# Kernel optimization log

Hardware: AMD Instinct MI355X
Metric: run time of the kernel (lower is better)

The kernel has to match this reference:

```python
import jax, jax.numpy as jnp
import numpy as np

B, H, S, D = 4, 16, 2048, 64
ROPE_BASE = 10000.0


def _rope(x):
    # Rotate-half RoPE over the last dim, positions along the second-to-last dim.
    d = x.shape[-1]
    s = x.shape[-2]
    inv_freq = 1.0 / (ROPE_BASE ** (jnp.arange(0, d, 2, dtype=jnp.float32) / d))  # [D/2]
    ang = jnp.arange(s, dtype=jnp.float32)[:, None] * inv_freq                    # [S, D/2]
    cos, sin = jnp.cos(ang), jnp.sin(ang)
    x1, x2 = x[..., : d // 2], x[..., d // 2:]
    return jnp.concatenate([x1 * cos - x2 * sin, x1 * sin + x2 * cos], axis=-1).astype(x.dtype)


def setup_inputs() -> dict:
    key = jax.random.key(0)
    kq, kk, kv = jax.random.split(key, 3)
    q = jax.random.normal(kq, (B, H, S, D), dtype=jnp.float32)
    k = jax.random.normal(kk, (B, H, S, D), dtype=jnp.float32)
    v = jax.random.normal(kv, (B, H, S, D), dtype=jnp.float32)
    mask = jnp.tril(jnp.ones((S, S), dtype=bool))  # causal, broadcasts over [B,H,S,S]
    return {"q": q, "k": k, "v": v, "mask": mask}


def reference(q, k, v, mask):
    d_k = q.shape[-1]
    qr = _rope(q)
    kr = _rope(k)
    scores = jnp.einsum('bhqd,bhkd->bhqk', qr, kr) / jnp.sqrt(jnp.asarray(d_k, jnp.float32))
    scores = jnp.where(mask, scores, -jnp.inf)  # masked_fill(mask == False, -inf)
    probs = jax.nn.softmax(scores, axis=-1)
    return jnp.einsum('bhqk,bhkd->bhqd', probs, v)
```

## Files before the change

### kernel.cpp

```cpp
#include <hip/hip_runtime.h>
#include <hip/hip_bf16.h>
#include <math.h>

#define SS 2048
#define DD 64
#define BH 64
#define KT 64
#define NT 256
#define NKT (SS / KT)
#define QTT 256
#define NTA 512
#define NQT (SS / QTT)
#define LQ 72
#define LOG2E 1.4426950408889634f
#define IFS (13.287712379549449f / 32.0f)

typedef __attribute__((ext_vector_type(8))) short s8v;
typedef __attribute__((ext_vector_type(4))) short s4v;
typedef __attribute__((ext_vector_type(4))) float f4v;

__device__ __forceinline__ short f2b(float x) {
  __hip_bfloat16 h = __float2bfloat16(x);
  return *reinterpret_cast<short*>(&h);
}

__device__ __forceinline__ void gload16(const void* g, void* l) {
  __builtin_amdgcn_global_load_lds(
      (const __attribute__((address_space(1))) void*)g,
      (__attribute__((address_space(3))) void*)l, 16, 0, 0);
}

template <int CTRL>
__device__ __forceinline__ float dppf(float x) {
  int i = __builtin_bit_cast(int, x);
  i = __builtin_amdgcn_update_dpp(i, i, CTRL, 0xf, 0xf, false);
  return __builtin_bit_cast(float, i);
}
__device__ __forceinline__ float rowmax16(float x) {
  x = fmaxf(x, dppf<0xB1>(x));
  x = fmaxf(x, dppf<0x4E>(x));
  x = fmaxf(x, dppf<0x124>(x));
  x = fmaxf(x, dppf<0x128>(x));
  return x;
}
__device__ __forceinline__ float rowsum16(float x) {
  x += dppf<0xB1>(x);
  x += dppf<0x4E>(x);
  x += dppf<0x124>(x);
  x += dppf<0x128>(x);
  return x;
}

__device__ __forceinline__ void rope_cs(int pos, int j, float& c, float& s) {
  float inv = exp2f(-(float)j * IFS);
  float ang = (float)pos * inv;
  __sincosf(ang, &s, &c);
}

__global__ __launch_bounds__(NT) void prep_kv_kernel(
    const float* __restrict__ kg, const float* __restrict__ vg,
    short* __restrict__ kr, short* __restrict__ vt) {
  __shared__ float Vs[KT][DD + 1];
  const int b = blockIdx.x;
  const int kt = b & 31;
  const int t = threadIdx.x;
  const size_t ofs = (size_t)b * (KT * DD);
  const float* ktile = kg + ofs;
  short* krt = kr + ofs;

#pragma unroll
  for (int i = 0; i < 8; ++i) {
    int idx = t + i * NT;
    int r = idx >> 5, j = idx & 31;
    float s, c;
    rope_cs(kt * KT + r, j, c, s);
    float x1 = ktile[r * DD + j], x2 = ktile[r * DD + j + 32];
    krt[r * DD + j] = f2b(x1 * c - x2 * s);
    krt[r * DD + j + 32] = f2b(x1 * s + x2 * c);
  }

  const float* vtile = vg + ofs;
#pragma unroll
  for (int i = 0; i < 4; ++i) {
    int s4 = t + i * NT;
    int r = s4 >> 4, c4 = (s4 & 15) * 4;
    float4 v = *(const float4*)&vtile[r * DD + c4];
    Vs[r][c4 + 0] = v.x;
    Vs[r][c4 + 1] = v.y;
    Vs[r][c4 + 2] = v.z;
    Vs[r][c4 + 3] = v.w;
  }
  __syncthreads();
  short* otile = vt + ofs;
#pragma unroll
  for (int i = 0; i < 2; ++i) {
    int c = t + i * NT;
    int d = c >> 3, k8 = (c & 7) * 8;
    s8v o;
#pragma unroll
    for (int u = 0; u < 8; ++u) {
      int kp = k8 + u;
      int src = ((kp & 3) << 4) + (kp >> 2);
      o[u] = f2b(Vs[src][d]);
    }
    *(s8v*)&otile[d * KT + k8] = o;
  }
}

__global__ __launch_bounds__(NTA, 4) void attn_fast(
    const float* __restrict__ qg, const short* __restrict__ kr,
    const short* __restrict__ vt, float* __restrict__ og) {
  __shared__ __align__(16) short Ks[2][KT * DD];
  __shared__ __align__(16) short Vts[2][DD * KT];
  __shared__ __align__(16) short QP[QTT * DD];

  const int tid = threadIdx.x;
  const int lane = tid & 63;
  const int wv = tid >> 6;
  const int quad = lane >> 4;
  const int lx = lane & 15;
  const int xb = lx & 7;
  const int foff0 = ((quad ^ xb) << 3);
  const int foff1 = (((quad | 4) ^ xb) << 3);

  const int bid = blockIdx.x;
  const int g = bid >> 6;
  const int qb = (g < 4) ? (7 - g) : (g - 4);
  const int bh = bid & 63;
  const int qbase = qb * QTT;
  const int ktmax = 4 * qb + 3;
  const int mykt = 4 * qb + (wv >> 1);
  const float* Q = qg + (size_t)bh * SS * DD;
  float* O = og + (size_t)bh * SS * DD;
  const short* krh = kr + (size_t)bh * SS * DD;
  const short* vth = vt + (size_t)bh * SS * DD;

  const int r_dma = tid >> 3;
  const int qs_dma = (tid & 7) ^ (r_dma & 7);
  const int goff = r_dma * DD + qs_dma * 8;
  const int loff = wv * 512;

  gload16(krh + goff, &Ks[0][loff]);
  gload16(vth + goff, &Vts[0][loff]);

  const float qscale = 0.125f * LOG2E;
#pragma unroll
  for (int t = 0; t < 16; ++t) {
    int idx = tid + t * NTA;
    int r = idx >> 5, j = idx & 31;
    float s, c;
    rope_cs(qbase + r, j, c, s);
    float x1 = Q[(size_t)(qbase + r) * DD + j];
    float x2 = Q[(size_t)(qbase + r) * DD + j + 32];
    int rb = r & 7;
    QP[r * DD + ((((j >> 3) ^ rb) << 3) | (j & 7))] = f2b((x1 * c - x2 * s) * qscale);
    QP[r * DD + (((((j >> 3) | 4) ^ rb) << 3) | (j & 7))] = f2b((x1 * s + x2 * c) * qscale);
  }
  __syncthreads();

  s8v qf0[2], qf1[2];
#pragma unroll
  for (int h = 0; h < 2; ++h) {
    const int rq = wv * 32 + h * 16 + lx;
    qf0[h] = *(const s8v*)&QP[rq * DD + foff0];
    qf1[h] = *(const s8v*)&QP[rq * DD + foff1];
  }

  const short bone = f2b(1.0f);
  s8v ones;
#pragma unroll
  for (int u = 0; u < 8; ++u) ones[u] = bone;

  short* Ps = &QP[wv * 32 * DD];

  f4v o_[2][4];
  f4v ol[2];
#pragma unroll
  for (int h = 0; h < 2; ++h) {
    ol[h] = (f4v){0.f, 0.f, 0.f, 0.f};
#pragma unroll
    for (int db = 0; db < 4; ++db) o_[h][db] = (f4v){0.f, 0.f, 0.f, 0.f};
  }

  for (int kt = 0; kt <= ktmax; ++kt) {
    const int cur = kt & 1;
    if (kt) __syncthreads();

    if (kt < ktmax) {
      const short* ktile = krh + (size_t)(kt + 1) * (KT * DD);
      const short* vtile = vth + (size_t)(kt + 1) * (DD * KT);
      const int nxt = cur ^ 1;
      gload16(ktile + goff, &Ks[nxt][loff]);
      gload16(vtile + goff, &Vts[nxt][loff]);
    }

    if (kt <= mykt) {
      f4v sc[2][4];
#pragma unroll
      for (int nb = 0; nb < 4; ++nb) {
        const int rk = nb * 16 + lx;
        s8v kf0 = *(const s8v*)&Ks[cur][rk * DD + foff0];
        s8v kf1 = *(const s8v*)&Ks[cur][rk * DD + foff1];
#pragma unroll
        for (int h = 0; h < 2; ++h) {
          f4v z = (f4v){0.f, 0.f, 0.f, 0.f};
          z = __builtin_amdgcn_mfma_f32_16x16x32_bf16(qf0[h], kf0, z, 0, 0, 0);
          z = __builtin_amdgcn_mfma_f32_16x16x32_bf16(qf1[h], kf1, z, 0, 0, 0);
          sc[h][nb] = z;
        }
      }

      if (kt == mykt) {
        const int kb = kt * KT;
#pragma unroll
        for (int h = 0; h < 2; ++h) {
          const int qrow = qbase + wv * 32 + h * 16 + quad * 4;
#pragma unroll
          for (int nb = 0; nb < 4; ++nb)
#pragma unroll
            for (int r = 0; r < 4; ++r)
              if (kb + nb * 16 + lx > qrow + r) sc[h][nb][r] = -INFINITY;
        }
      }

#pragma unroll
      for (int h = 0; h < 2; ++h) {
#pragma unroll
        for (int r = 0; r < 4; ++r) {
          const int rl = quad * 4 + r;
          float p0 = __builtin_amdgcn_exp2f(sc[h][0][r]);
          float p1 = __builtin_amdgcn_exp2f(sc[h][1][r]);
          float p2 = __builtin_amdgcn_exp2f(sc[h][2][r]);
          float p3 = __builtin_amdgcn_exp2f(sc[h][3][r]);
          s4v pk = {f2b(p0), f2b(p1), f2b(p2), f2b(p3)};
          *(s4v*)&Ps[(h * 16 + rl) * DD + (((lx >> 1) ^ (rl & 7)) << 3) + ((lx & 1) << 2)] = pk;
        }
      }

      s8v pf0[2], pf1[2];
#pragma unroll
      for (int h = 0; h < 2; ++h) {
        pf0[h] = *(const s8v*)&Ps[(h * 16 + lx) * DD + foff0];
        pf1[h] = *(const s8v*)&Ps[(h * 16 + lx) * DD + foff1];
        ol[h] = __builtin_amdgcn_mfma_f32_16x16x32_bf16(pf0[h], ones, ol[h], 0, 0, 0);
        ol[h] = __builtin_amdgcn_mfma_f32_16x16x32_bf16(pf1[h], ones, ol[h], 0, 0, 0);
      }
#pragma unroll
      for (int db = 0; db < 4; ++db) {
        const int rv = db * 16 + lx;
        s8v vf0 = *(const s8v*)&Vts[cur][rv * KT + foff0];
        s8v vf1 = *(const s8v*)&Vts[cur][rv * KT + foff1];
#pragma unroll
        for (int h = 0; h < 2; ++h) {
          o_[h][db] = __builtin_amdgcn_mfma_f32_16x16x32_bf16(pf0[h], vf0, o_[h][db], 0, 0, 0);
          o_[h][db] = __builtin_amdgcn_mfma_f32_16x16x32_bf16(pf1[h], vf1, o_[h][db], 0, 0, 0);
        }
      }
    }
  }

#pragma unroll
  for (int h = 0; h < 2; ++h)
#pragma unroll
    for (int r = 0; r < 4; ++r) {
      float rinv = 1.0f / ol[h][r];
      int row = qbase + wv * 32 + h * 16 + quad * 4 + r;
#pragma unroll
      for (int db = 0; db < 4; ++db)
        O[(size_t)row * DD + db * 16 + lx] = o_[h][db][r] * rinv;
    }
}

__global__ __launch_bounds__(NT, 4) void attn_fallback(
    const float* __restrict__ qg, const float* __restrict__ kg,
    const float* __restrict__ vg, float* __restrict__ og) {
  __shared__ __align__(16) short Qs[64 * LQ];
  __shared__ __align__(16) short Ksh[64 * LQ];
  __shared__ __align__(16) short Vt[DD * LQ];
  __shared__ __align__(16) short Ps[4][16 * LQ];

  const int tid = threadIdx.x;
  const int lane = tid & 63;
  const int wv = tid >> 6;
  const int quad = lane >> 4;
  const int lx = lane & 15;

  const int bid = blockIdx.x;
  const int qt = NKT - 1 - (bid >> 6);
  const int bh = bid & 63;
  const int qbase = qt * 64;
  const size_t base = (size_t)bh * SS * DD;
  const float* Q = qg + base;
  const float* K = kg + base;
  const float* V = vg + base;
  float* O = og + base;

  const float qscale = 0.125f * LOG2E;
  for (int t = 0; t < 8; ++t) {
    int idx = tid + t * NT;
    int r = idx >> 5, j = idx & 31;
    float c, s;
    rope_cs(qbase + r, j, c, s);
    float x1 = Q[(size_t)(qbase + r) * DD + j];
    float x2 = Q[(size_t)(qbase + r) * DD + j + 32];
    Qs[r * LQ + j] = f2b((x1 * c - x2 * s) * qscale);
    Qs[r * LQ + j + 32] = f2b((x1 * s + x2 * c) * qscale);
  }
  __syncthreads();

  s8v qf0 = *(const s8v*)&Qs[(wv * 16 + lx) * LQ + quad * 8];
  s8v qf1 = *(const s8v*)&Qs[(wv * 16 + lx) * LQ + 32 + quad * 8];

  float m_[4], l_[4];
  f4v o_[4];
#pragma unroll
  for (int r = 0; r < 4; ++r) { m_[r] = -INFINITY; l_[r] = 0.f; }
#pragma unroll
  for (int db = 0; db < 4; ++db) o_[db] = (f4v){0.f, 0.f, 0.f, 0.f};

  for (int kt = 0; kt <= qt; ++kt) {
    const int kbase = kt * 64;
    __syncthreads();
    for (int t = 0; t < 8; ++t) {
      int idx = tid + t * NT;
      int r = idx >> 5, j = idx & 31;
      float c, s;
      rope_cs(kbase + r, j, c, s);
      float x1 = K[(size_t)(kbase + r) * DD + j];
      float x2 = K[(size_t)(kbase + r) * DD + j + 32];
      Ksh[r * LQ + j] = f2b(x1 * c - x2 * s);
      Ksh[r * LQ + j + 32] = f2b(x1 * s + x2 * c);
    }
    for (int t = 0; t < 4; ++t) {
      int i4 = tid + t * NT;
      int r = i4 >> 4, c4 = (i4 & 15) * 4;
      const float4 v = *(const float4*)&V[(size_t)(kbase + r) * DD + c4];
      Vt[(c4 + 0) * LQ + r] = f2b(v.x);
      Vt[(c4 + 1) * LQ + r] = f2b(v.y);
      Vt[(c4 + 2) * LQ + r] = f2b(v.z);
      Vt[(c4 + 3) * LQ + r] = f2b(v.w);
    }
    __syncthreads();

    f4v sc[4];
#pragma unroll
    for (int nb = 0; nb < 4; ++nb) {
      s8v kf0 = *(const s8v*)&Ksh[(nb * 16 + lx) * LQ + quad * 8];
      s8v kf1 = *(const s8v*)&Ksh[(nb * 16 + lx) * LQ + 32 + quad * 8];
      f4v z = (f4v){0.f, 0.f, 0.f, 0.f};
      z = __builtin_amdgcn_mfma_f32_16x16x32_bf16(qf0, kf0, z, 0, 0, 0);
      z = __builtin_amdgcn_mfma_f32_16x16x32_bf16(qf1, kf1, z, 0, 0, 0);
      sc[nb] = z;
    }
    if (kt == qt) {
#pragma unroll
      for (int nb = 0; nb < 4; ++nb)
#pragma unroll
        for (int r = 0; r < 4; ++r)
          if (kbase + nb * 16 + lx > qbase + wv * 16 + quad * 4 + r)
            sc[nb][r] = -INFINITY;
    }
#pragma unroll
    for (int r = 0; r < 4; ++r) {
      float mx = fmaxf(fmaxf(sc[0][r], sc[1][r]), fmaxf(sc[2][r], sc[3][r]));
      mx = rowmax16(mx);
      float mn = fmaxf(m_[r], mx);
      float al = __builtin_amdgcn_exp2f(m_[r] - mn);
      m_[r] = mn;
      float rs = 0.f;
#pragma unroll
      for (int nb = 0; nb < 4; ++nb) {
        float p = __builtin_amdgcn_exp2f(sc[nb][r] - mn);
        rs += p;
        Ps[wv][(quad * 4 + r) * LQ + nb * 16 + lx] = f2b(p);
      }
      rs = rowsum16(rs);
      l_[r] = l_[r] * al + rs;
      o_[0][r] *= al; o_[1][r] *= al; o_[2][r] *= al; o_[3][r] *= al;
    }
    s8v pf0 = *(const s8v*)&Ps[wv][lx * LQ + quad * 8];
    s8v pf1 = *(const s8v*)&Ps[wv][lx * LQ + 32 + quad * 8];
#pragma unroll
    for (int db = 0; db < 4; ++db) {
      s8v vf0 = *(const s8v*)&Vt[(db * 16 + lx) * LQ + quad * 8];
      s8v vf1 = *(const s8v*)&Vt[(db * 16 + lx) * LQ + 32 + quad * 8];
      o_[db] = __builtin_amdgcn_mfma_f32_16x16x32_bf16(pf0, vf0, o_[db], 0, 0, 0);
      o_[db] = __builtin_amdgcn_mfma_f32_16x16x32_bf16(pf1, vf1, o_[db], 0, 0, 0);
    }
  }
#pragma unroll
  for (int r = 0; r < 4; ++r) {
    float rinv = 1.0f / l_[r];
    int row = qbase + wv * 16 + quad * 4 + r;
#pragma unroll
    for (int db = 0; db < 4; ++db)
      O[(size_t)row * DD + db * 16 + lx] = o_[db][r] * rinv;
  }
}

extern "C" void kernel_launch(void* const* d_in, const int* in_sizes, int n_in,
                              void* d_out, int out_size, void* d_ws, size_t ws_size,
                              hipStream_t stream) {
  const float* q = (const float*)d_in[0];
  const float* k = (const float*)d_in[1];
  const float* v = (const float*)d_in[2];
  float* out = (float*)d_out;

  const size_t kr_bytes = (size_t)BH * SS * DD * sizeof(short);
  const size_t vt_bytes = kr_bytes;
  const size_t need = kr_bytes + vt_bytes;

  if (ws_size >= need) {
    short* kr = (short*)d_ws;
    short* vt = (short*)((char*)d_ws + kr_bytes);
    prep_kv_kernel<<<BH * NKT, NT, 0, stream>>>(k, v, kr, vt);
    attn_fast<<<dim3(BH * NQT), dim3(NTA), 0, stream>>>(q, kr, vt, out);
  } else {
    attn_fallback<<<dim3(BH * NKT), dim3(NT), 0, stream>>>(q, k, v, out);
  }
}
```

Before: 186.1 us.

## Pair causal query tiles per block and keep softmax probabilities in registers

The attention kernel now uses 128-row query tiles and 256 threads. Each block processes a complementary pair of tiles (15-g and g), so every block runs the same fixed number of K/V iterations and causal load is balanced. The QK product is computed transposed (K as the A operand), so the exp'd scores already sit in the MFMA A-operand layout. This removes the LDS round trip for P, and the V-transpose prep kernel permutes keys to match. It adds a mid-loop tile switch with an output flush, and launch bounds drop to 2 blocks per SM.

```diff
diff --git a/kernel.cpp b/kernel.cpp
--- a/kernel.cpp
+++ b/kernel.cpp
@@ -8,9 +8,9 @@
 #define KT 64
 #define NT 256
 #define NKT (SS / KT)
-#define QTT 256
-#define NTA 512
-#define NQT (SS / QTT)
+#define QTT 128
+#define NTA 256
+#define NPAIR 8
 #define LQ 72
 #define LOG2E 1.4426950408889634f
 #define IFS (13.287712379549449f / 32.0f)
@@ -100,19 +100,20 @@
 #pragma unroll
     for (int u = 0; u < 8; ++u) {
       int kp = k8 + u;
-      int src = ((kp & 3) << 4) + (kp >> 2);
+      int src = ((kp & 31) >> 3) * 4 + (kp & 3) +
+                ((kp >> 5) * 2 + ((kp >> 2) & 1)) * 16;
       o[u] = f2b(Vs[src][d]);
     }
     *(s8v*)&otile[d * KT + k8] = o;
   }
 }
 
-__global__ __launch_bounds__(NTA, 4) void attn_fast(
+__global__ __launch_bounds__(NTA, 2) void attn_fast(
     const float* __restrict__ qg, const short* __restrict__ kr,
     const short* __restrict__ vt, float* __restrict__ og) {
   __shared__ __align__(16) short Ks[2][KT * DD];
   __shared__ __align__(16) short Vts[2][DD * KT];
-  __shared__ __align__(16) short QP[QTT * DD];
+  __shared__ __align__(16) short QQ[2][QTT * DD];
 
   const int tid = threadIdx.x;
   const int lane = tid & 63;
@@ -125,45 +126,53 @@
 
   const int bid = blockIdx.x;
   const int g = bid >> 6;
-  const int qb = (g < 4) ? (7 - g) : (g - 4);
   const int bh = bid & 63;
-  const int qbase = qb * QTT;
-  const int ktmax = 4 * qb + 3;
-  const int mykt = 4 * qb + (wv >> 1);
+  const int qbA = 15 - g;
+  const int qbB = g;
   const float* Q = qg + (size_t)bh * SS * DD;
   float* O = og + (size_t)bh * SS * DD;
   const short* krh = kr + (size_t)bh * SS * DD;
   const short* vth = vt + (size_t)bh * SS * DD;
 
-  const int r_dma = tid >> 3;
-  const int qs_dma = (tid & 7) ^ (r_dma & 7);
-  const int goff = r_dma * DD + qs_dma * 8;
-  const int loff = wv * 512;
-
-  gload16(krh + goff, &Ks[0][loff]);
-  gload16(vth + goff, &Vts[0][loff]);
+  int goff[2], loff[2];
+#pragma unroll
+  for (int i = 0; i < 2; ++i) {
+    int c = wv * 128 + i * 64 + lane;
+    int r = c >> 3, qp = c & 7;
+    int qs = qp ^ (r & 7);
+    goff[i] = r * DD + qs * 8;
+    loff[i] = (wv * 128 + i * 64) * 8;
+  }
+
+#pragma unroll
+  for (int i = 0; i < 2; ++i) {
+    gload16(krh + goff[i], &Ks[0][loff[i]]);
+    gload16(vth + goff[i], &Vts[0][loff[i]]);
+  }
 
   const float qscale = 0.125f * LOG2E;
-#pragma unroll
-  for (int t = 0; t < 16; ++t) {
+  for (int t = 0; t < 32; ++t) {
     int idx = tid + t * NTA;
     int r = idx >> 5, j = idx & 31;
+    int ph = r >> 7, rr = r & 127;
+    int grow = (ph ? qbB : qbA) * QTT + rr;
     float s, c;
-    rope_cs(qbase + r, j, c, s);
-    float x1 = Q[(size_t)(qbase + r) * DD + j];
-    float x2 = Q[(size_t)(qbase + r) * DD + j + 32];
-    int rb = r & 7;
-    QP[r * DD + ((((j >> 3) ^ rb) << 3) | (j & 7))] = f2b((x1 * c - x2 * s) * qscale);
-    QP[r * DD + (((((j >> 3) | 4) ^ rb) << 3) | (j & 7))] = f2b((x1 * s + x2 * c) * qscale);
+    rope_cs(grow, j, c, s);
+    float x1 = Q[(size_t)grow * DD + j];
+    float x2 = Q[(size_t)grow * DD + j + 32];
+    short* dst = &QQ[ph][0];
+    int rb = rr & 7;
+    dst[rr * DD + ((((j >> 3) ^ rb) << 3) | (j & 7))] = f2b((x1 * c - x2 * s) * qscale);
+    dst[rr * DD + (((((j >> 3) | 4) ^ rb) << 3) | (j & 7))] = f2b((x1 * s + x2 * c) * qscale);
   }
   __syncthreads();
 
-  s8v qf0[2], qf1[2];
+  s8v qx0[2], qx1[2];
 #pragma unroll
   for (int h = 0; h < 2; ++h) {
     const int rq = wv * 32 + h * 16 + lx;
-    qf0[h] = *(const s8v*)&QP[rq * DD + foff0];
-    qf1[h] = *(const s8v*)&QP[rq * DD + foff1];
+    qx0[h] = *(const s8v*)&QQ[0][rq * DD + foff0];
+    qx1[h] = *(const s8v*)&QQ[0][rq * DD + foff1];
   }
 
   const short bone = f2b(1.0f);
@@ -171,8 +180,6 @@
 #pragma unroll
   for (int u = 0; u < 8; ++u) ones[u] = bone;
 
-  short* Ps = &QP[wv * 32 * DD];
-
   f4v o_[2][4];
   f4v ol[2];
 #pragma unroll
@@ -182,16 +189,25 @@
     for (int db = 0; db < 4; ++db) o_[h][db] = (f4v){0.f, 0.f, 0.f, 0.f};
   }
 
-  for (int kt = 0; kt <= ktmax; ++kt) {
-    const int cur = kt & 1;
-    if (kt) __syncthreads();
-
-    if (kt < ktmax) {
-      const short* ktile = krh + (size_t)(kt + 1) * (KT * DD);
-      const short* vtile = vth + (size_t)(kt + 1) * (DD * KT);
-      const int nxt = cur ^ 1;
-      gload16(ktile + goff, &Ks[nxt][loff]);
-      gload16(vtile + goff, &Vts[nxt][loff]);
+  int qb = qbA;
+  int ktend = 2 * qbA + 1;
+  int mykt = 2 * qbA + (wv >> 1);
+  int kt = 0;
+  const int NIT = 34;
+
+  for (int it = 0; it < NIT; ++it) {
+    const int cur = it & 1;
+    __syncthreads();
+
+    if (it < NIT - 1) {
+      const int nt = (kt < ktend) ? kt + 1 : 0;
+      const short* ktile = krh + (size_t)nt * (KT * DD);
+      const short* vtile = vth + (size_t)nt * (DD * KT);
+#pragma unroll
+      for (int i = 0; i < 2; ++i) {
+        gload16(ktile + goff[i], &Ks[cur ^ 1][loff[i]]);
+        gload16(vtile + goff[i], &Vts[cur ^ 1][loff[i]]);
+      }
     }
 
     if (kt <= mykt) {
@@ -204,47 +220,39 @@
 #pragma unroll
         for (int h = 0; h < 2; ++h) {
           f4v z = (f4v){0.f, 0.f, 0.f, 0.f};
-          z = __builtin_amdgcn_mfma_f32_16x16x32_bf16(qf0[h], kf0, z, 0, 0, 0);
-          z = __builtin_amdgcn_mfma_f32_16x16x32_bf16(qf1[h], kf1, z, 0, 0, 0);
+          z = __builtin_amdgcn_mfma_f32_16x16x32_bf16(kf0, qx0[h], z, 0, 0, 0);
+          z = __builtin_amdgcn_mfma_f32_16x16x32_bf16(kf1, qx1[h], z, 0, 0, 0);
           sc[h][nb] = z;
         }
       }
 
       if (kt == mykt) {
-        const int kb = kt * KT;
 #pragma unroll
         for (int h = 0; h < 2; ++h) {
-          const int qrow = qbase + wv * 32 + h * 16 + quad * 4;
+          const int thr = (wv & 1) * 32 + h * 16 + lx;
 #pragma unroll
           for (int nb = 0; nb < 4; ++nb)
 #pragma unroll
             for (int r = 0; r < 4; ++r)
-              if (kb + nb * 16 + lx > qrow + r) sc[h][nb][r] = -INFINITY;
+              if (nb * 16 + quad * 4 + r > thr) sc[h][nb][r] = -INFINITY;
         }
       }
 
+      s8v pf0[2], pf1[2];
 #pragma unroll
       for (int h = 0; h < 2; ++h) {
 #pragma unroll
-        for (int r = 0; r < 4; ++r) {
-          const int rl = quad * 4 + r;
-          float p0 = __builtin_amdgcn_exp2f(sc[h][0][r]);
-          float p1 = __builtin_amdgcn_exp2f(sc[h][1][r]);
-          float p2 = __builtin_amdgcn_exp2f(sc[h][2][r]);
-          float p3 = __builtin_amdgcn_exp2f(sc[h][3][r]);
-          s4v pk = {f2b(p0), f2b(p1), f2b(p2), f2b(p3)};
-          *(s4v*)&Ps[(h * 16 + rl) * DD + (((lx >> 1) ^ (rl & 7)) << 3) + ((lx & 1) << 2)] = pk;
-        }
-      }
-
-      s8v pf0[2], pf1[2];
-#pragma unroll
-      for (int h = 0; h < 2; ++h) {
-        pf0[h] = *(const s8v*)&Ps[(h * 16 + lx) * DD + foff0];
-        pf1[h] = *(const s8v*)&Ps[(h * 16 + lx) * DD + foff1];
+        for (int nb = 0; nb < 4; ++nb)
+#pragma unroll
+          for (int r = 0; r < 4; ++r) {
+            short pb = f2b(__builtin_amdgcn_exp2f(sc[h][nb][r]));
+            if (nb < 2) pf0[h][nb * 4 + r] = pb;
+            else        pf1[h][(nb - 2) * 4 + r] = pb;
+          }
         ol[h] = __builtin_amdgcn_mfma_f32_16x16x32_bf16(pf0[h], ones, ol[h], 0, 0, 0);
         ol[h] = __builtin_amdgcn_mfma_f32_16x16x32_bf16(pf1[h], ones, ol[h], 0, 0, 0);
       }
+
 #pragma unroll
       for (int db = 0; db < 4; ++db) {
         const int rv = db * 16 + lx;
@@ -257,6 +265,33 @@
         }
       }
     }
+
+    ++kt;
+    if (kt > ktend && it < NIT - 1) {
+#pragma unroll
+      for (int h = 0; h < 2; ++h)
+#pragma unroll
+        for (int r = 0; r < 4; ++r) {
+          float rinv = 1.0f / ol[h][r];
+          int row = qb * QTT + wv * 32 + h * 16 + quad * 4 + r;
+#pragma unroll
+          for (int db = 0; db < 4; ++db)
+            O[(size_t)row * DD + db * 16 + lx] = o_[h][db][r] * rinv;
+        }
+#pragma unroll
+      for (int h = 0; h < 2; ++h) {
+        ol[h] = (f4v){0.f, 0.f, 0.f, 0.f};
+#pragma unroll
+        for (int db = 0; db < 4; ++db) o_[h][db] = (f4v){0.f, 0.f, 0.f, 0.f};
+        const int rq = wv * 32 + h * 16 + lx;
+        qx0[h] = *(const s8v*)&QQ[1][rq * DD + foff0];
+        qx1[h] = *(const s8v*)&QQ[1][rq * DD + foff1];
+      }
+      qb = qbB;
+      ktend = 2 * qbB + 1;
+      mykt = 2 * qbB + (wv >> 1);
+      kt = 0;
+    }
   }
 
 #pragma unroll
@@ -264,7 +299,7 @@
 #pragma unroll
     for (int r = 0; r < 4; ++r) {
       float rinv = 1.0f / ol[h][r];
-      int row = qbase + wv * 32 + h * 16 + quad * 4 + r;
+      int row = qb * QTT + wv * 32 + h * 16 + quad * 4 + r;
 #pragma unroll
       for (int db = 0; db < 4; ++db)
         O[(size_t)row * DD + db * 16 + lx] = o_[h][db][r] * rinv;
@@ -414,7 +449,7 @@
     short* kr = (short*)d_ws;
     short* vt = (short*)((char*)d_ws + kr_bytes);
     prep_kv_kernel<<<BH * NKT, NT, 0, stream>>>(k, v, kr, vt);
-    attn_fast<<<dim3(BH * NQT), dim3(NTA), 0, stream>>>(q, kr, vt, out);
+    attn_fast<<<dim3(BH * NPAIR), dim3(NTA), 0, stream>>>(q, kr, vt, out);
   } else {
     attn_fallback<<<dim3(BH * NKT), dim3(NT), 0, stream>>>(q, k, v, out);
   }
```

Measured after the change: 186.6 us. About the same (+0.3%).
